# Kernel optimization log

Measured on AMD Instinct MI355X. Metric: run time of the kernel, lower is better.

The kernel has to match this reference:

```python
import jax, jax.numpy as jnp
import numpy as np

S, B, D, H, HD = 2048, 1, 1280, 16, 80
NSEQ = 8  # packed sequences

def setup_inputs() -> dict:
    key = jax.random.key(0)
    k1, k2, k3 = jax.random.split(key, 3)
    x = jax.random.normal(k1, (S, B, D), dtype=jnp.float32)
    # cu_seqlens: 8 equal packed segments, starts at 0, ends at S
    cu_seqlens = (jnp.arange(NSEQ + 1, dtype=jnp.int32) * (S // NSEQ))
    W_qkv = jax.random.normal(k2, (3 * D, D), dtype=jnp.float32) * (1.0 / np.sqrt(D))
    b_qkv = jax.random.normal(k3, (3 * D,), dtype=jnp.float32) * 0.01
    return {"x": x, "cu_seqlens": cu_seqlens, "W_qkv": W_qkv, "b_qkv": b_qkv}

def _block_diag_mask(cu_seqlens, s):
    # segment id of each position; positions in the same segment attend to each other
    pos = jnp.arange(s)
    seg = jnp.searchsorted(cu_seqlens[1:], pos, side='right')  # [s]
    return seg[:, None] == seg[None, :]  # [s, s] bool

def reference(x, cu_seqlens, W_qkv, b_qkv):
    s, b, d = x.shape
    qkv = jnp.einsum('sbd,ed->sbe', x, W_qkv) + b_qkv  # [s,b,3d]
    q, k, v = jnp.split(qkv, 3, axis=2)
    # [s,b,h,hd] -> [b,h,s,hd]
    def to_bhsd(t):
        return t.reshape(s, b, H, HD).transpose(1, 2, 0, 3)
    q1, k1, v1 = to_bhsd(q), to_bhsd(k), to_bhsd(v)
    mask = _block_diag_mask(cu_seqlens, s)  # [s,s]
    scale = 1.0 / np.sqrt(HD)
    scores = jnp.einsum('bhsd,bhtd->bhst', q1, k1) * scale  # [b,h,s,s]
    neg = jnp.finfo(scores.dtype).min
    scores = jnp.where(mask[None, None, :, :], scores, neg)
    attn = jax.nn.softmax(scores, axis=-1)
    out = jnp.einsum('bhst,bhtd->bhsd', attn, v1)  # [b,h,s,hd]
    return out.transpose(0, 2, 1, 3)  # [b,s,h,hd]
```

## Files before the change

### kernel.cpp

```cpp
#include <hip/hip_runtime.h>
#include <hip/hip_bf16.h>

#define S_LEN 2048
#define DIM 1280
#define NH 16
#define HD 80
#define NE 3840
#define SEG 256
#define NSEG 8
#define QKV_SZ (NH * S_LEN * HD)
#define NX (S_LEN * DIM)
#define NW (NE * DIM)

typedef short short8 __attribute__((ext_vector_type(8)));
typedef float floatx4 __attribute__((ext_vector_type(4)));

__device__ inline unsigned short f2bf(float f) {
    unsigned int u = __float_as_uint(f);
    return (unsigned short)((u + 0x7fffu + ((u >> 16) & 1u)) >> 16);
}

__global__ __launch_bounds__(256) void convert_bf16_kernel(
    const float* __restrict__ x, const float* __restrict__ W,
    unsigned short* __restrict__ xb, unsigned short* __restrict__ Wb)
{
    const int gi = blockIdx.x * 256 + threadIdx.x;
    const float* src;
    unsigned short* dst;
    int off;
    if (gi < NX / 4) { src = x; dst = xb; off = gi * 4; }
    else             { src = W; dst = Wb; off = (gi - NX / 4) * 4; }
    float4 v = *(const float4*)(src + off);
    ushort4 o;
    o.x = f2bf(v.x); o.y = f2bf(v.y); o.z = f2bf(v.z); o.w = f2bf(v.w);
    *(ushort4*)(dst + off) = o;
}

__global__ __launch_bounds__(256, 4) void qkv_gemm_kernel(
    const unsigned short* __restrict__ xb,
    const unsigned short* __restrict__ Wb,
    const float* __restrict__ bias,
    unsigned short* __restrict__ qkvb)
{
    __shared__ short SMEM[64 * 136];
    short* As = SMEM;
    short* Bs = SMEM + 4096;
    short* Vt = SMEM;

    const int tid  = threadIdx.x;
    const int w    = tid >> 6;
    const int lane = tid & 63;
    const int m0 = blockIdx.y * 128;
    const int n0 = blockIdx.x * 64;

    const int row16 = lane >> 2;
    const int kgl   = lane & 3;
    const int kswz  = 8 * (kgl ^ ((row16 >> 1) & 3));
    const int ra0 = 16 * w + row16;
    const int ra1 = 64 + 16 * w + row16;
    const unsigned short* agp0 = xb + (size_t)(m0 + ra0) * DIM + kswz;
    const unsigned short* agp1 = xb + (size_t)(m0 + ra1) * DIM + kswz;
    const unsigned short* bgp  = Wb + (size_t)(n0 + ra0) * DIM + kswz;
    short* alp0 = &As[ra0 * 32 + kgl * 8];
    short* alp1 = &As[ra1 * 32 + kgl * 8];
    short* blp  = &Bs[ra0 * 32 + kgl * 8];

    const int quad = lane >> 4;
    const int lm   = lane & 15;
    const int ko   = 8 * (quad ^ ((lm >> 1) & 3));
    const int warow = w * 32;

    floatx4 acc[2][4];
    #pragma unroll
    for (int i = 0; i < 2; ++i)
        #pragma unroll
        for (int j = 0; j < 4; ++j)
            acc[i][j] = (floatx4){0.f, 0.f, 0.f, 0.f};

    for (int k0 = 0; k0 < DIM; k0 += 32) {
        __syncthreads();
        __builtin_amdgcn_global_load_lds(
            (const __attribute__((address_space(1))) unsigned int*)(agp0 + k0),
            (__attribute__((address_space(3))) unsigned int*)alp0, 16, 0, 0);
        __builtin_amdgcn_global_load_lds(
            (const __attribute__((address_space(1))) unsigned int*)(agp1 + k0),
            (__attribute__((address_space(3))) unsigned int*)alp1, 16, 0, 0);
        __builtin_amdgcn_global_load_lds(
            (const __attribute__((address_space(1))) unsigned int*)(bgp + k0),
            (__attribute__((address_space(3))) unsigned int*)blp, 16, 0, 0);
        __syncthreads();

        short8 a[2], b[4];
        #pragma unroll
        for (int i = 0; i < 2; ++i)
            a[i] = *(const short8*)&As[(warow + i * 16 + lm) * 32 + ko];
        #pragma unroll
        for (int j = 0; j < 4; ++j)
            b[j] = *(const short8*)&Bs[(j * 16 + lm) * 32 + ko];
        #pragma unroll
        for (int i = 0; i < 2; ++i)
            #pragma unroll
            for (int j = 0; j < 4; ++j)
                acc[i][j] = __builtin_amdgcn_mfma_f32_16x16x32_bf16(
                    a[i], b[j], acc[i][j], 0, 0, 0);
    }

    const int which = n0 / DIM;
    const int nrem0 = n0 - which * DIM;

    if (which < 2) {
        #pragma unroll
        for (int j = 0; j < 4; ++j) {
            const int nrem = nrem0 + j * 16 + lm;
            const float bv = bias[which * DIM + nrem];
            const int hh = nrem / HD;
            const int hd = nrem - hh * HD;
            unsigned short* hp = qkvb + (size_t)which * QKV_SZ
                               + (size_t)hh * (S_LEN * HD) + hd;
            #pragma unroll
            for (int i = 0; i < 2; ++i) {
                const int mbase = m0 + warow + i * 16 + quad * 4;
                #pragma unroll
                for (int r = 0; r < 4; ++r)
                    hp[(size_t)(mbase + r) * HD] = f2bf(acc[i][j][r] + bv);
            }
        }
    } else {
        unsigned short* Vg = qkvb + 2 * (size_t)QKV_SZ;
        __syncthreads();
        #pragma unroll
        for (int j = 0; j < 4; ++j) {
            const int nn = j * 16 + lm;
            const float bv = bias[2 * DIM + nrem0 + nn];
            #pragma unroll
            for (int i = 0; i < 2; ++i) {
                const int mloc = warow + i * 16 + quad * 4;
                #pragma unroll
                for (int t = 0; t < 2; ++t) {
                    const unsigned pk =
                        ((unsigned)f2bf(acc[i][j][2 * t + 1] + bv) << 16)
                      | (unsigned)f2bf(acc[i][j][2 * t] + bv);
                    *(unsigned*)&Vt[nn * 136 + mloc + 2 * t] = pk;
                }
            }
        }
        __syncthreads();
        #pragma unroll
        for (int rnd = 0; rnd < 4; ++rnd) {
            const int f = rnd * 256 + tid;
            const int nn = f >> 4;
            const int mg = f & 15;
            const int nrem = nrem0 + nn;
            const int hhh = nrem / HD;
            const int hd = nrem - hhh * HD;
            unsigned short* gp = Vg + (size_t)hhh * (HD * S_LEN)
                               + (size_t)hd * S_LEN + m0 + mg * 8;
            *(short8*)gp = *(const short8*)&Vt[nn * 136 + mg * 8];
        }
    }
}

__global__ __launch_bounds__(256) void attn_kernel(
    const unsigned short* __restrict__ Qb,
    const unsigned short* __restrict__ Kb,
    const unsigned short* __restrict__ Vb,
    float* __restrict__ out)
{
    __shared__ short KVs[128 * 104];
    __shared__ short Ps[32 * 136];
    __shared__ float rsl[4][32];

    const int qc  = blockIdx.x;
    const int h   = blockIdx.y;
    const int seg = blockIdx.z;
    const int tid = threadIdx.x;
    const int w    = tid >> 6;
    const int lane = tid & 63;
    const int quad = lane >> 4;
    const int lm   = lane & 15;
    const int qbase = seg * SEG + qc * 32;
    const float scale = 0.11180339887498948f;
    const short8 zfrag = {0, 0, 0, 0, 0, 0, 0, 0};

    short8 aQ[2][3];
    #pragma unroll
    for (int mt = 0; mt < 2; ++mt) {
        const unsigned short* qp = Qb + ((size_t)h * S_LEN + qbase + mt * 16 + lm) * HD;
        #pragma unroll
        for (int ks = 0; ks < 3; ++ks) {
            const int hd0 = ks * 32 + quad * 8;
            aQ[mt][ks] = (hd0 < 80) ? *(const short8*)(qp + hd0) : zfrag;
        }
    }

    const int mtile  = w >> 1;
    const int ntbase = (w & 1) ? 3 : 0;
    const int ntcnt  = (w & 1) ? 2 : 3;

    floatx4 Oacc[3];
    #pragma unroll
    for (int t = 0; t < 3; ++t) Oacc[t] = (floatx4){0.f, 0.f, 0.f, 0.f};
    float rsp[2][4];
    #pragma unroll
    for (int mt = 0; mt < 2; ++mt)
        #pragma unroll
        for (int r = 0; r < 4; ++r) rsp[mt][r] = 0.0f;

    for (int half = 0; half < 2; ++half) {
        const int k0g = seg * SEG + half * 128;

        __syncthreads();
        {
            const unsigned short* src = Kb + ((size_t)h * S_LEN + k0g) * HD;
            #pragma unroll
            for (int rnd = 0; rnd < 5; ++rnd) {
                const int f = rnd * 256 + tid;
                const int key = f / 10;
                const int c = f - key * 10;
                *(short8*)&KVs[key * 104 + c * 8] = *(const short8*)(src + key * 80 + c * 8);
            }
            const int zkey = tid >> 1;
            const int zc = tid & 1;
            *(short8*)&KVs[zkey * 104 + 80 + zc * 8] = zfrag;
        }
        __syncthreads();

        floatx4 Cs[2][2];
        #pragma unroll
        for (int mt = 0; mt < 2; ++mt)
            #pragma unroll
            for (int nt = 0; nt < 2; ++nt) Cs[mt][nt] = (floatx4){0.f, 0.f, 0.f, 0.f};

        #pragma unroll
        for (int ks = 0; ks < 3; ++ks) {
            short8 b[2];
            #pragma unroll
            for (int nt = 0; nt < 2; ++nt)
                b[nt] = *(const short8*)&KVs[(w * 32 + nt * 16 + lm) * 104 + ks * 32 + quad * 8];
            #pragma unroll
            for (int mt = 0; mt < 2; ++mt)
                #pragma unroll
                for (int nt = 0; nt < 2; ++nt)
                    Cs[mt][nt] = __builtin_amdgcn_mfma_f32_16x16x32_bf16(
                        aQ[mt][ks], b[nt], Cs[mt][nt], 0, 0, 0);
        }

        #pragma unroll
        for (int mt = 0; mt < 2; ++mt)
            #pragma unroll
            for (int nt = 0; nt < 2; ++nt)
                #pragma unroll
                for (int r = 0; r < 4; ++r) {
                    const float p = __expf(Cs[mt][nt][r] * scale);
                    rsp[mt][r] += p;
                    const float po = __shfl_xor(p, 1);
                    if ((lm & 1) == 0) {
                        const unsigned pk = ((unsigned)f2bf(po) << 16) | (unsigned)f2bf(p);
                        *(unsigned*)&Ps[(mt * 16 + quad * 4 + r) * 136 + w * 32 + nt * 16 + lm] = pk;
                    }
                }
        __syncthreads();

        {
            const unsigned short* src = Vb + (size_t)h * (HD * S_LEN) + k0g;
            #pragma unroll
            for (int rnd = 0; rnd < 5; ++rnd) {
                const int f = rnd * 256 + tid;
                const int hd = f >> 4;
                const int sc = f & 15;
                *(short8*)&KVs[hd * 136 + sc * 8] = *(const short8*)(src + hd * S_LEN + sc * 8);
            }
        }
        __syncthreads();

        #pragma unroll
        for (int ks2 = 0; ks2 < 4; ++ks2) {
            const short8 a = *(const short8*)&Ps[(mtile * 16 + lm) * 136 + ks2 * 32 + quad * 8];
            #pragma unroll
            for (int t = 0; t < 3; ++t) {
                if (t < ntcnt) {
                    const int nt = ntbase + t;
                    const short8 b = *(const short8*)&KVs[(nt * 16 + lm) * 136 + ks2 * 32 + quad * 8];
                    Oacc[t] = __builtin_amdgcn_mfma_f32_16x16x32_bf16(a, b, Oacc[t], 0, 0, 0);
                }
            }
        }
    }

    #pragma unroll
    for (int mt = 0; mt < 2; ++mt)
        #pragma unroll
        for (int r = 0; r < 4; ++r) {
            float v = rsp[mt][r];
            v += __shfl_xor(v, 1);
            v += __shfl_xor(v, 2);
            v += __shfl_xor(v, 4);
            v += __shfl_xor(v, 8);
            if (lm == 0) rsl[w][mt * 16 + quad * 4 + r] = v;
        }
    __syncthreads();

    #pragma unroll
    for (int r = 0; r < 4; ++r) {
        const int row = mtile * 16 + quad * 4 + r;
        const float l = rsl[0][row] + rsl[1][row] + rsl[2][row] + rsl[3][row];
        const float linv = 1.0f / l;
        float* op = out + (size_t)(qbase + row) * (NH * HD) + h * HD;
        #pragma unroll
        for (int t = 0; t < 3; ++t)
            if (t < ntcnt)
                op[(ntbase + t) * 16 + lm] = Oacc[t][r] * linv;
    }
}

extern "C" void kernel_launch(void* const* d_in, const int* in_sizes, int n_in,
                              void* d_out, int out_size, void* d_ws, size_t ws_size,
                              hipStream_t stream)
{
    const float* x      = (const float*)d_in[0];
    const float* W_qkv  = (const float*)d_in[2];
    const float* b_qkv  = (const float*)d_in[3];
    float* out = (float*)d_out;

    unsigned short* xb = (unsigned short*)d_ws;
    unsigned short* Wb = xb + NX;
    unsigned short* qkvb = Wb + NW;
    unsigned short* Qb = qkvb;
    unsigned short* Kb = qkvb + QKV_SZ;
    unsigned short* Vb = qkvb + 2 * (size_t)QKV_SZ;

    convert_bf16_kernel<<<(NX + NW) / 4 / 256, 256, 0, stream>>>(x, W_qkv, xb, Wb);
    qkv_gemm_kernel<<<dim3(NE / 64, S_LEN / 128), 256, 0, stream>>>(xb, Wb, b_qkv, qkvb);
    attn_kernel<<<dim3(8, NH, NSEG), 256, 0, stream>>>(Qb, Kb, Vb, out);
}
```

Baseline: 139.7 us.

## Load QKV GEMM operands directly from global into registers with double buffering

Replaces the LDS-staged tile loads (global_load_lds plus two barriers per k-step) in the QKV projection GEMM with direct per-lane 16-byte global loads into MFMA operand registers. Two register sets alternate so the next k-slice is fetched while the current one feeds the MFMAs. This removes the per-iteration barriers and LDS traffic, but each wave now reads its operands itself, so B tiles are fetched redundantly by all four waves and register pressure rises; the occupancy hint in launch bounds is also dropped.

```diff
diff --git a/kernel.cpp b/kernel.cpp
--- a/kernel.cpp
+++ b/kernel.cpp
@@ -36,16 +36,13 @@
     *(ushort4*)(dst + off) = o;
 }
 
-__global__ __launch_bounds__(256, 4) void qkv_gemm_kernel(
+__global__ __launch_bounds__(256) void qkv_gemm_kernel(
     const unsigned short* __restrict__ xb,
     const unsigned short* __restrict__ Wb,
     const float* __restrict__ bias,
     unsigned short* __restrict__ qkvb)
 {
-    __shared__ short SMEM[64 * 136];
-    short* As = SMEM;
-    short* Bs = SMEM + 4096;
-    short* Vt = SMEM;
+    __shared__ short Vt[64 * 136];
 
     const int tid  = threadIdx.x;
     const int w    = tid >> 6;
@@ -53,22 +50,16 @@
     const int m0 = blockIdx.y * 128;
     const int n0 = blockIdx.x * 64;
 
-    const int row16 = lane >> 2;
-    const int kgl   = lane & 3;
-    const int kswz  = 8 * (kgl ^ ((row16 >> 1) & 3));
-    const int ra0 = 16 * w + row16;
-    const int ra1 = 64 + 16 * w + row16;
-    const unsigned short* agp0 = xb + (size_t)(m0 + ra0) * DIM + kswz;
-    const unsigned short* agp1 = xb + (size_t)(m0 + ra1) * DIM + kswz;
-    const unsigned short* bgp  = Wb + (size_t)(n0 + ra0) * DIM + kswz;
-    short* alp0 = &As[ra0 * 32 + kgl * 8];
-    short* alp1 = &As[ra1 * 32 + kgl * 8];
-    short* blp  = &Bs[ra0 * 32 + kgl * 8];
-
     const int quad = lane >> 4;
     const int lm   = lane & 15;
-    const int ko   = 8 * (quad ^ ((lm >> 1) & 3));
     const int warow = w * 32;
+
+    const unsigned short* pa0 = xb + (size_t)(m0 + warow + lm) * DIM + quad * 8;
+    const unsigned short* pa1 = pa0 + (size_t)16 * DIM;
+    const unsigned short* pb0 = Wb + (size_t)(n0 + lm) * DIM + quad * 8;
+    const unsigned short* pb1 = pb0 + (size_t)16 * DIM;
+    const unsigned short* pb2 = pb0 + (size_t)32 * DIM;
+    const unsigned short* pb3 = pb0 + (size_t)48 * DIM;
 
     floatx4 acc[2][4];
     #pragma unroll
@@ -77,33 +68,40 @@
         for (int j = 0; j < 4; ++j)
             acc[i][j] = (floatx4){0.f, 0.f, 0.f, 0.f};
 
-    for (int k0 = 0; k0 < DIM; k0 += 32) {
-        __syncthreads();
-        __builtin_amdgcn_global_load_lds(
-            (const __attribute__((address_space(1))) unsigned int*)(agp0 + k0),
-            (__attribute__((address_space(3))) unsigned int*)alp0, 16, 0, 0);
-        __builtin_amdgcn_global_load_lds(
-            (const __attribute__((address_space(1))) unsigned int*)(agp1 + k0),
-            (__attribute__((address_space(3))) unsigned int*)alp1, 16, 0, 0);
-        __builtin_amdgcn_global_load_lds(
-            (const __attribute__((address_space(1))) unsigned int*)(bgp + k0),
-            (__attribute__((address_space(3))) unsigned int*)blp, 16, 0, 0);
-        __syncthreads();
-
-        short8 a[2], b[4];
-        #pragma unroll
-        for (int i = 0; i < 2; ++i)
-            a[i] = *(const short8*)&As[(warow + i * 16 + lm) * 32 + ko];
-        #pragma unroll
-        for (int j = 0; j < 4; ++j)
-            b[j] = *(const short8*)&Bs[(j * 16 + lm) * 32 + ko];
-        #pragma unroll
-        for (int i = 0; i < 2; ++i)
-            #pragma unroll
-            for (int j = 0; j < 4; ++j)
-                acc[i][j] = __builtin_amdgcn_mfma_f32_16x16x32_bf16(
-                    a[i], b[j], acc[i][j], 0, 0, 0);
-    }
+    short8 s0a0, s0a1, s0b0, s0b1, s0b2, s0b3;
+    short8 s1a0, s1a1, s1b0, s1b1, s1b2, s1b3;
+
+#define LDSET(p, koff)                                   \
+    p##a0 = *(const short8*)(pa0 + (koff));              \
+    p##a1 = *(const short8*)(pa1 + (koff));              \
+    p##b0 = *(const short8*)(pb0 + (koff));              \
+    p##b1 = *(const short8*)(pb1 + (koff));              \
+    p##b2 = *(const short8*)(pb2 + (koff));              \
+    p##b3 = *(const short8*)(pb3 + (koff));
+
+#define MMSET(p)                                                             \
+    acc[0][0] = __builtin_amdgcn_mfma_f32_16x16x32_bf16(p##a0, p##b0, acc[0][0], 0, 0, 0); \
+    acc[0][1] = __builtin_amdgcn_mfma_f32_16x16x32_bf16(p##a0, p##b1, acc[0][1], 0, 0, 0); \
+    acc[0][2] = __builtin_amdgcn_mfma_f32_16x16x32_bf16(p##a0, p##b2, acc[0][2], 0, 0, 0); \
+    acc[0][3] = __builtin_amdgcn_mfma_f32_16x16x32_bf16(p##a0, p##b3, acc[0][3], 0, 0, 0); \
+    acc[1][0] = __builtin_amdgcn_mfma_f32_16x16x32_bf16(p##a1, p##b0, acc[1][0], 0, 0, 0); \
+    acc[1][1] = __builtin_amdgcn_mfma_f32_16x16x32_bf16(p##a1, p##b1, acc[1][1], 0, 0, 0); \
+    acc[1][2] = __builtin_amdgcn_mfma_f32_16x16x32_bf16(p##a1, p##b2, acc[1][2], 0, 0, 0); \
+    acc[1][3] = __builtin_amdgcn_mfma_f32_16x16x32_bf16(p##a1, p##b3, acc[1][3], 0, 0, 0);
+
+    LDSET(s0, 0)
+    for (int k0 = 0; k0 < DIM - 64; k0 += 64) {
+        LDSET(s1, k0 + 32)
+        MMSET(s0)
+        LDSET(s0, k0 + 64)
+        MMSET(s1)
+    }
+    LDSET(s1, DIM - 32)
+    MMSET(s0)
+    MMSET(s1)
+
+#undef LDSET
+#undef MMSET
 
     const int which = n0 / DIM;
     const int nrem0 = n0 - which * DIM;
@@ -127,7 +125,6 @@
         }
     } else {
         unsigned short* Vg = qkvb + 2 * (size_t)QKV_SZ;
-        __syncthreads();
         #pragma unroll
         for (int j = 0; j < 4; ++j) {
             const int nn = j * 16 + lm;
```

New measurement: 210.5 us. +50.6%, slower.
